# Kernel optimization log

Hardware: AMD Instinct MI355X
Metric: run time of the kernel (lower is better)

## Reference

```python
import jax, jax.numpy as jnp
import numpy as np
import math

B, L, HID = 2, 2048, 1024
H, DK, RATIO, SHARED, TOPK = 4, 64, 4, 1, 2
EXP_V = 2
DV = DK * EXP_V
KEY_DIM = H * DK
VAL_DIM = KEY_DIM * EXP_V
HE = H * RATIO
KS = 4
EPS = 1e-5


def _silu(x):
    return x * jax.nn.sigmoid(x)


def _dwconv_causal(x, w):
    # x: (B, L, C), w: (C, KS); causal depthwise short conv
    xp = jnp.pad(x, ((0, 0), (KS - 1, 0), (0, 0))).transpose(0, 2, 1)
    y = jax.lax.conv_general_dilated(xp, w[:, None, :], (1,), 'VALID',
                                     feature_group_count=w.shape[0],
                                     dimension_numbers=('NCH', 'OIH', 'NCH'))
    return y.transpose(0, 2, 1)


def _l2norm(x):
    return x * jax.lax.rsqrt(jnp.sum(x * x, -1, keepdims=True) + 1e-6)


def _forward(hidden_states, Wq, Wk, Wv, Wb, Wa, Wg, Wo, conv_q, conv_k, conv_v,
             Wq_exp, Wk_exp, W_gate, A_log, dt_bias, norm_w):
    x = hidden_states
    q = _silu(_dwconv_causal(x @ Wq.T, conv_q)).reshape(B, L, H, DK)
    k = _silu(_dwconv_causal(x @ Wk.T, conv_k)).reshape(B, L, H, DK)
    v = _silu(_dwconv_causal(x @ Wv.T, conv_v)).reshape(B, L, H, DV)
    # per-head expert expansion -> (B,L,H,RATIO,DK)
    qe = jnp.einsum('blhd,hkd->blhk', q, Wq_exp).reshape(B, L, H, RATIO, DK)
    ke = jnp.einsum('blhd,hkd->blhk', k, Wk_exp).reshape(B, L, H, RATIO, DK)
    qe = _l2norm(qe) * (DK ** -0.5)
    ke = _l2norm(ke)
    # token-policy top-k routing over non-shared experts
    logits = jnp.einsum('blhd,nd->blhn', q, W_gate)
    scores = jax.nn.softmax(logits.astype(jnp.float32), axis=-1)
    tw, ti = jax.lax.top_k(scores, TOPK)
    tw = tw / jnp.sum(tw, -1, keepdims=True)
    full = jnp.sum(jax.nn.one_hot(ti + SHARED, RATIO, dtype=tw.dtype) * tw[..., None], axis=-2)
    full = full.at[..., :SHARED].set(1.0 / SHARED)
    w_r = (full / jnp.sum(full, -1, keepdims=True)).astype(x.dtype)  # (B,L,H,RATIO)
    mask = (w_r > 0).astype(x.dtype)
    beta = jax.nn.sigmoid(x @ Wb.T).reshape(B, L, H, RATIO) * mask
    g = -jnp.exp(A_log).reshape(H, RATIO) * jax.nn.softplus((x @ Wa.T) + dt_bias).reshape(B, L, H, RATIO)
    g = g * mask  # unrouted memories: exp(0)=1, no decay, no update
    # gated delta-rule recurrence over HE = H*RATIO memories
    qs = qe.reshape(B, L, HE, DK).transpose(1, 0, 2, 3)
    ks_ = ke.reshape(B, L, HE, DK).transpose(1, 0, 2, 3)
    vs = jnp.broadcast_to(v[:, :, :, None, :], (B, L, H, RATIO, DV)).reshape(B, L, HE, DV).transpose(1, 0, 2, 3)
    bs = beta.reshape(B, L, HE).transpose(1, 0, 2)
    gs = g.reshape(B, L, HE).transpose(1, 0, 2)

    def step(S, xs):
        qt, kt, vt, bt, gt = xs
        S = S * jnp.exp(gt)[..., None, None]
        kv = jnp.einsum('bhk,bhkv->bhv', kt, S)
        S = S + jnp.einsum('bhk,bhv->bhkv', kt, (vt - kv) * bt[..., None])
        return S, jnp.einsum('bhk,bhkv->bhv', qt, S)

    S0 = jnp.zeros((B, HE, DK, DV), x.dtype)
    _, o = jax.lax.scan(step, S0, (qs, ks_, vs, bs, gs))
    o = o.transpose(1, 0, 2, 3).reshape(B, L, H, RATIO, DV)
    o = jnp.einsum('blhe,blhev->blhv', w_r, o)
    # FusedRMSNormSwishGate + output projection
    gate = (x @ Wg.T).reshape(B, L, H, DV)
    o = o * jax.lax.rsqrt(jnp.mean(o * o, -1, keepdims=True) + EPS) * norm_w * _silu(gate)
    return o.reshape(B, L, VAL_DIM) @ Wo.T


def setup_inputs():
    keys = jax.random.split(jax.random.key(0), 18)
    n = lambda i, shp, sc=1.0: jax.random.normal(keys[i], shp, jnp.float32) * sc
    A = jax.random.uniform(keys[14], (HE,), jnp.float32, 1e-3, 16.0)
    dt = jnp.exp(jax.random.uniform(keys[15], (HE,), jnp.float32) * (math.log(0.1) - math.log(0.001)) + math.log(0.001))
    dt = jnp.clip(dt, 1e-4, None)
    return {
        'hidden_states': n(0, (B, L, HID)),
        'Wq': n(1, (KEY_DIM, HID), HID ** -0.5),
        'Wk': n(2, (KEY_DIM, HID), HID ** -0.5),
        'Wv': n(3, (VAL_DIM, HID), HID ** -0.5),
        'Wb': n(4, (HE, HID), HID ** -0.5),
        'Wa': n(5, (HE, HID), HID ** -0.5),
        'Wg': n(6, (VAL_DIM, HID), HID ** -0.5),
        'Wo': n(7, (HID, VAL_DIM), VAL_DIM ** -0.5),
        'conv_q': n(8, (KEY_DIM, KS), 0.5),
        'conv_k': n(9, (KEY_DIM, KS), 0.5),
        'conv_v': n(10, (VAL_DIM, KS), 0.5),
        'Wq_exp': n(11, (H, RATIO * DK, DK), DK ** -0.5),
        'Wk_exp': n(12, (H, RATIO * DK, DK), DK ** -0.5),
        'W_gate': n(13, (RATIO - SHARED, DK), DK ** -0.5),
        'A_log': jnp.log(A),
        'dt_bias': dt + jnp.log(-jnp.expm1(-dt)),
        'norm_w': jnp.ones((DV,), jnp.float32),
    }


def reference(hidden_states, Wq, Wk, Wv, Wb, Wa, Wg, Wo, conv_q, conv_k, conv_v,
              Wq_exp, Wk_exp, W_gate, A_log, dt_bias, norm_w):
    return _forward(hidden_states, Wq, Wk, Wv, Wb, Wa, Wg, Wo, conv_q, conv_k, conv_v,
                    Wq_exp, Wk_exp, W_gate, A_log, dt_bias, norm_w)
```

## Files before the change

kernel.cpp:

```cpp
#include <hip/hip_runtime.h>
#include <hip/hip_bf16.h>
#include <math.h>

#define B_    2
#define L_    2048
#define HID_  1024
#define H_    4
#define DK_   64
#define RATIO_ 4
#define HE_   16
#define DV_   128
#define T_    64
#define NC_   32
#define SPITCH 72
#define APITCH 68
#define NCAT  1408
#define QMP   68
#define QMSZ  4352

typedef __attribute__((ext_vector_type(8))) short short8;
typedef __attribute__((ext_vector_type(4))) float f32x4;

__device__ __forceinline__ float sigmoidf_(float x){ return 1.f/(1.f+expf(-x)); }
__device__ __forceinline__ ushort f2bf(float x){
  __hip_bfloat16 h = __float2bfloat16(x);
  return *reinterpret_cast<ushort*>(&h);
}
__device__ __forceinline__ float bf2f(ushort u){
  union { uint32_t i; float f; } v; v.i = ((uint32_t)u) << 16; return v.f;
}

__global__ __launch_bounds__(256) void cast_bf16(const float* __restrict__ in,
                                                 ushort* __restrict__ out, int n)
{
  int i = blockIdx.x*256 + threadIdx.x;
  if (i < n) out[i] = f2bf(in[i]);
}

__global__ __launch_bounds__(256) void concat_wcat(const float* __restrict__ Wk,
    const float* __restrict__ Wv, const float* __restrict__ Wg,
    const float* __restrict__ Wb, const float* __restrict__ Wa,
    ushort* __restrict__ Wcat)
{
  int idx = blockIdx.x*256 + threadIdx.x;
  if (idx >= NCAT*1024) return;
  int r = idx >> 10, cc = idx & 1023;
  float v = 0.f;
  if      (r < 256)  v = Wk[(size_t)r*1024 + cc];
  else if (r < 768)  v = Wv[(size_t)(r-256)*1024 + cc];
  else if (r < 1280) v = Wg[(size_t)(r-768)*1024 + cc];
  else if (r < 1296) v = Wb[(size_t)(r-1280)*1024 + cc];
  else if (r < 1312) v = Wa[(size_t)(r-1296)*1024 + cc];
  Wcat[idx] = f2bf(v);
}

__global__ __launch_bounds__(256) void gemm_bf16(
    const ushort* __restrict__ A, int lda,
    const ushort* __restrict__ Bm, int ldb,
    float* __restrict__ C, int ldc, int K)
{
  __shared__ ushort As[128*32];
  __shared__ ushort Bs[128*32];
  const int tid  = threadIdx.x;
  const int wave = tid >> 6, lane = tid & 63;
  const int row0 = blockIdx.y*128, col0 = blockIdx.x*128;
  const int wr = (wave >> 1) * 64, wc = (wave & 1) * 64;
  const int frow = lane & 15;
  const int fko  = (lane >> 4) << 3;
  f32x4 acc[4][4];
  #pragma unroll
  for (int i=0;i<4;i++)
    #pragma unroll
    for (int j=0;j<4;j++) acc[i][j] = (f32x4){0.f,0.f,0.f,0.f};
  for (int k0 = 0; k0 < K; k0 += 32) {
    #pragma unroll
    for (int cc = 0; cc < 2; cc++) {
      int c  = wave*128 + cc*64 + lane;
      int r  = c >> 2;
      int ko = (c & 3) << 3;
      __builtin_amdgcn_global_load_lds(
        (const __attribute__((address_space(1))) void*)(A + (size_t)(row0+r)*lda + k0 + ko),
        (__attribute__((address_space(3))) void*)(As + (size_t)(wave*128 + cc*64)*8),
        16, 0, 0);
      __builtin_amdgcn_global_load_lds(
        (const __attribute__((address_space(1))) void*)(Bm + (size_t)(col0+r)*ldb + k0 + ko),
        (__attribute__((address_space(3))) void*)(Bs + (size_t)(wave*128 + cc*64)*8),
        16, 0, 0);
    }
    __syncthreads();
    short8 af[4], bfv[4];
    #pragma unroll
    for (int mi=0;mi<4;mi++)
      af[mi] = *reinterpret_cast<const short8*>(&As[(wr + mi*16 + frow)*32 + fko]);
    #pragma unroll
    for (int ni=0;ni<4;ni++)
      bfv[ni] = *reinterpret_cast<const short8*>(&Bs[(wc + ni*16 + frow)*32 + fko]);
    #pragma unroll
    for (int mi=0;mi<4;mi++)
      #pragma unroll
      for (int ni=0;ni<4;ni++)
        acc[mi][ni] = __builtin_amdgcn_mfma_f32_16x16x32_bf16(af[mi], bfv[ni], acc[mi][ni], 0, 0, 0);
    __syncthreads();
  }
  const int ocol = lane & 15;
  const int orow = (lane >> 4) << 2;
  #pragma unroll
  for (int mi=0;mi<4;mi++)
    #pragma unroll
    for (int ni=0;ni<4;ni++) {
      size_t base = (size_t)(row0 + wr + mi*16 + orow)*ldc + (col0 + wc + ni*16 + ocol);
      #pragma unroll
      for (int q=0;q<4;q++) C[base + (size_t)q*ldc] = acc[mi][ni][q];
    }
}

__global__ __launch_bounds__(256) void gemm_expand_bf16(
    const ushort* __restrict__ qc_bf, const ushort* __restrict__ kc_bf,
    const ushort* __restrict__ Wqeb, const ushort* __restrict__ Wkeb,
    ushort* __restrict__ qeb, ushort* __restrict__ keb)
{
  const int z = blockIdx.z;
  const int hh = z & 3;
  const ushort* A  = (z < 4 ? qc_bf : kc_bf) + hh*64;
  const ushort* Bm = (z < 4 ? Wqeb  : Wkeb ) + (size_t)hh*16384;
  ushort* C        = (z < 4 ? qeb   : keb  ) + hh*256;
  const int lda = 256, ldb = 64, ldc = 1024, K = 64;
  __shared__ ushort As[128*32];
  __shared__ ushort Bs[128*32];
  const int tid  = threadIdx.x;
  const int wave = tid >> 6, lane = tid & 63;
  const int row0 = blockIdx.y*128, col0 = blockIdx.x*128;
  const int wr = (wave >> 1) * 64, wc = (wave & 1) * 64;
  const int frow = lane & 15;
  const int fko  = (lane >> 4) << 3;
  f32x4 acc[4][4];
  #pragma unroll
  for (int i=0;i<4;i++)
    #pragma unroll
    for (int j=0;j<4;j++) acc[i][j] = (f32x4){0.f,0.f,0.f,0.f};
  for (int k0 = 0; k0 < K; k0 += 32) {
    #pragma unroll
    for (int cc = 0; cc < 2; cc++) {
      int c  = wave*128 + cc*64 + lane;
      int r  = c >> 2;
      int ko = (c & 3) << 3;
      __builtin_amdgcn_global_load_lds(
        (const __attribute__((address_space(1))) void*)(A + (size_t)(row0+r)*lda + k0 + ko),
        (__attribute__((address_space(3))) void*)(As + (size_t)(wave*128 + cc*64)*8),
        16, 0, 0);
      __builtin_amdgcn_global_load_lds(
        (const __attribute__((address_space(1))) void*)(Bm + (size_t)(col0+r)*ldb + k0 + ko),
        (__attribute__((address_space(3))) void*)(Bs + (size_t)(wave*128 + cc*64)*8),
        16, 0, 0);
    }
    __syncthreads();
    short8 af[4], bfv[4];
    #pragma unroll
    for (int mi=0;mi<4;mi++)
      af[mi] = *reinterpret_cast<const short8*>(&As[(wr + mi*16 + frow)*32 + fko]);
    #pragma unroll
    for (int ni=0;ni<4;ni++)
      bfv[ni] = *reinterpret_cast<const short8*>(&Bs[(wc + ni*16 + frow)*32 + fko]);
    #pragma unroll
    for (int mi=0;mi<4;mi++)
      #pragma unroll
      for (int ni=0;ni<4;ni++)
        acc[mi][ni] = __builtin_amdgcn_mfma_f32_16x16x32_bf16(af[mi], bfv[ni], acc[mi][ni], 0, 0, 0);
    __syncthreads();
  }
  const int ocol = lane & 15;
  const int orow = (lane >> 4) << 2;
  #pragma unroll
  for (int mi=0;mi<4;mi++)
    #pragma unroll
    for (int ni=0;ni<4;ni++) {
      size_t base = (size_t)(row0 + wr + mi*16 + orow)*ldc + (col0 + wc + ni*16 + ocol);
      #pragma unroll
      for (int q=0;q<4;q++) C[base + (size_t)q*ldc] = f2bf(acc[mi][ni][q]);
    }
}

__global__ __launch_bounds__(256) void gemm_f32_db(const float* __restrict__ A, int lda,
    const float* __restrict__ Bm, int ldb, float* __restrict__ C, int ldc,
    int M, int N, int K)
{
  __shared__ float As[2][32][64];
  __shared__ float Bs[2][32][64];
  const int tid = threadIdx.x;
  const int row0 = blockIdx.y * 64;
  const int col0 = blockIdx.x * 64;
  const int tx = tid & 15, ty = tid >> 4;
  const int r0s = tid >> 3;
  const int k4s = (tid & 7) << 2;
  float4 av0, av1, bv0, bv1;

  av0 = *(const float4*)&A[(size_t)(row0 + r0s)*lda + k4s];
  av1 = *(const float4*)&A[(size_t)(row0 + r0s + 32)*lda + k4s];
  bv0 = (col0 + r0s < N) ? *(const float4*)&Bm[(size_t)(col0 + r0s)*ldb + k4s] : make_float4(0,0,0,0);
  bv1 = (col0 + r0s + 32 < N) ? *(const float4*)&Bm[(size_t)(col0 + r0s + 32)*ldb + k4s] : make_float4(0,0,0,0);
  As[0][k4s+0][r0s] = av0.x; As[0][k4s+1][r0s] = av0.y; As[0][k4s+2][r0s] = av0.z; As[0][k4s+3][r0s] = av0.w;
  As[0][k4s+0][r0s+32] = av1.x; As[0][k4s+1][r0s+32] = av1.y; As[0][k4s+2][r0s+32] = av1.z; As[0][k4s+3][r0s+32] = av1.w;
  Bs[0][k4s+0][r0s] = bv0.x; Bs[0][k4s+1][r0s] = bv0.y; Bs[0][k4s+2][r0s] = bv0.z; Bs[0][k4s+3][r0s] = bv0.w;
  Bs[0][k4s+0][r0s+32] = bv1.x; Bs[0][k4s+1][r0s+32] = bv1.y; Bs[0][k4s+2][r0s+32] = bv1.z; Bs[0][k4s+3][r0s+32] = bv1.w;
  __syncthreads();

  float acc[4][4] = {};
  const int nt = K >> 5;
  for (int kt = 0; kt < nt; ++kt) {
    const int p = kt & 1;
    if (kt + 1 < nt) {
      int k0 = (kt+1) << 5;
      av0 = *(const float4*)&A[(size_t)(row0 + r0s)*lda + k0 + k4s];
      av1 = *(const float4*)&A[(size_t)(row0 + r0s + 32)*lda + k0 + k4s];
      bv0 = (col0 + r0s < N) ? *(const float4*)&Bm[(size_t)(col0 + r0s)*ldb + k0 + k4s] : make_float4(0,0,0,0);
      bv1 = (col0 + r0s + 32 < N) ? *(const float4*)&Bm[(size_t)(col0 + r0s + 32)*ldb + k0 + k4s] : make_float4(0,0,0,0);
    }
    #pragma unroll
    for (int kk = 0; kk < 32; kk++) {
      float4 a4 = *(const float4*)&As[p][kk][ty*4];
      float4 b4 = *(const float4*)&Bs[p][kk][tx*4];
      float a[4] = {a4.x,a4.y,a4.z,a4.w};
      float b[4] = {b4.x,b4.y,b4.z,b4.w};
      #pragma unroll
      for (int i=0;i<4;i++)
        #pragma unroll
        for (int j=0;j<4;j++) acc[i][j] += a[i]*b[j];
    }
    if (kt + 1 < nt) {
      const int q = p ^ 1;
      As[q][k4s+0][r0s] = av0.x; As[q][k4s+1][r0s] = av0.y; As[q][k4s+2][r0s] = av0.z; As[q][k4s+3][r0s] = av0.w;
      As[q][k4s+0][r0s+32] = av1.x; As[q][k4s+1][r0s+32] = av1.y; As[q][k4s+2][r0s+32] = av1.z; As[q][k4s+3][r0s+32] = av1.w;
      Bs[q][k4s+0][r0s] = bv0.x; Bs[q][k4s+1][r0s] = bv0.y; Bs[q][k4s+2][r0s] = bv0.z; Bs[q][k4s+3][r0s] = bv0.w;
      Bs[q][k4s+0][r0s+32] = bv1.x; Bs[q][k4s+1][r0s+32] = bv1.y; Bs[q][k4s+2][r0s+32] = bv1.z; Bs[q][k4s+3][r0s+32] = bv1.w;
    }
    __syncthreads();
  }
  #pragma unroll
  for (int i=0;i<4;i++) {
    int r = row0 + ty*4 + i;
    #pragma unroll
    for (int j=0;j<4;j++) {
      int cc = col0 + tx*4 + j;
      if (cc < N) C[(size_t)r*ldc + cc] = acc[i][j];
    }
  }
}

__global__ __launch_bounds__(256) void conv_silu(const float* __restrict__ in, int ild,
    const float* __restrict__ w, float* __restrict__ outf, ushort* __restrict__ outb,
    int C, int total)
{
  int n = blockIdx.x*256 + threadIdx.x;
  if (n >= total) return;
  int c = n % C;
  int t = (n / C) % L_;
  int b = n / (C*L_);
  float acc = 0.f;
  #pragma unroll
  for (int s = 0; s < 4; s++) {
    int tt = t - 3 + s;
    if (tt >= 0) acc += in[((size_t)b*L_ + tt)*ild + c] * w[c*4+s];
  }
  float y = acc * sigmoidf_(acc);
  if (outf) outf[n] = y;
  if (outb) outb[n] = f2bf(y);
}

__global__ __launch_bounds__(256) void routing(const float* __restrict__ qc,
    const float* __restrict__ kvgba, const float* __restrict__ Wg3,
    const float* __restrict__ A_log, const float* __restrict__ dt_bias,
    float* __restrict__ w_buf, float* __restrict__ bt_buf, float* __restrict__ g_buf)
{
  int n = blockIdx.x*256 + threadIdx.x;
  int h  = n & 3;
  int bl = n >> 2;
  const float* q = qc + (size_t)bl*256 + h*64;
  float l0=0.f, l1=0.f, l2=0.f;
  for (int d=0; d<64; d++) {
    float qd = q[d];
    l0 += qd*Wg3[d]; l1 += qd*Wg3[64+d]; l2 += qd*Wg3[128+d];
  }
  float mx = fmaxf(l0, fmaxf(l1, l2));
  float e0 = expf(l0-mx), e1 = expf(l1-mx), e2 = expf(l2-mx);
  float inv_s = 1.f/(e0+e1+e2);
  float p0 = e0*inv_s, p1 = e1*inv_s, p2 = e2*inv_s;
  int m1 = 0; float pm1 = p0;
  if (p1 > pm1) { m1 = 1; pm1 = p1; }
  if (p2 > pm1) { m1 = 2; pm1 = p2; }
  int ia = (m1==0) ? 1 : 0;
  int ib = (m1==2) ? 1 : 2;
  float pa = (m1==0) ? p1 : p0;
  float pb = (m1==2) ? p1 : p2;
  int   m2  = (pb > pa) ? ib : ia;
  float pm2 = (pb > pa) ? pb : pa;
  float inv_w = 1.f/(pm1 + pm2);
  float w1 = 0.5f*pm1*inv_w;
  float w2 = 0.5f*pm2*inv_w;
  #pragma unroll
  for (int r = 0; r < 4; r++) {
    float wr = (r==0) ? 0.5f : (((r-1)==m1) ? w1 : (((r-1)==m2) ? w2 : 0.f));
    int he = h*4 + r;
    size_t gi = (size_t)bl*16 + he;
    w_buf[gi] = wr;
    float mask = (wr > 0.f) ? 1.f : 0.f;
    bt_buf[gi] = mask * sigmoidf_(kvgba[(size_t)bl*NCAT + 1280 + he]);
    float av = kvgba[(size_t)bl*NCAT + 1296 + he] + dt_bias[he];
    float sp = fmaxf(av, 0.f) + log1pf(expf(-fabsf(av)));
    g_buf[gi] = -expf(A_log[he]) * sp * mask;
  }
}

__global__ __launch_bounds__(256) void l2norm_rows_bf(ushort* __restrict__ v, float scale)
{
  int row  = blockIdx.x*4 + (threadIdx.x >> 6);
  int lane = threadIdx.x & 63;
  size_t idx = (size_t)row*64 + lane;
  float x = bf2f(v[idx]);
  float ss = x*x;
  #pragma unroll
  for (int off = 32; off > 0; off >>= 1) ss += __shfl_xor(ss, off);
  v[idx] = f2bf(x * rsqrtf(ss + 1e-6f) * scale);
}

__device__ __forceinline__ f32x4 tile64(const ushort* Am, int r0,
                                        const ushort* Bm, int c0, int lane)
{
  f32x4 acc = {0.f,0.f,0.f,0.f};
  const int fr = lane & 15, fo = (lane >> 4) << 3;
  #pragma unroll
  for (int kk = 0; kk < 2; ++kk) {
    short8 a = *reinterpret_cast<const short8*>(&Am[(r0+fr)*SPITCH + fo + kk*32]);
    short8 b = *reinterpret_cast<const short8*>(&Bm[(c0+fr)*SPITCH + fo + kk*32]);
    acc = __builtin_amdgcn_mfma_f32_16x16x32_bf16(a, b, acc, 0, 0, 0);
  }
  return acc;
}

__global__ __launch_bounds__(256,2) void scan_chunk_mfma(
    const ushort* __restrict__ keb, const ushort* __restrict__ qeb,
    const float* __restrict__ vc, const float* __restrict__ bt_buf,
    const float* __restrict__ g_buf, float* __restrict__ o_r,
    float* __restrict__ Qt, float* __restrict__ Mc, float* __restrict__ Bc)
{
  __shared__ float smem[18496];
  ushort* Kbf = (ushort*)smem;
  ushort* Qbf = (ushort*)(smem + 2304);
  ushort* KTD = (ushort*)(smem + 4608);
  float*  Af  = smem + 6912;
  ushort* Pf  = (ushort*)(smem + 6912);
  ushort* UV  = (ushort*)(smem + 11264);
  float*  cgs = smem + 18176;
  float*  bts = cgs + 64;
  float*  bGs = bts + 64;
  float*  Ds  = bGs + 64;
  float*  gams= Ds + 64;

  const int id = blockIdx.x;
  const int c   = id >> 5;
  const int bhe = id & 31;
  const int b  = bhe >> 4;
  const int he = bhe & 15;
  const int h = he >> 2;
  const int tid = threadIdx.x;
  const int wave = tid >> 6, lane = tid & 63;
  const size_t l0 = (size_t)b*L_ + (size_t)c*T_;

  const int tr = tid >> 2;
  const int sg = tid & 3;
  uint32_t kwv[8], qwv[8];
  float4 vreg[8];
  {
    const uint4* kp = (const uint4*)(keb + (l0+tr)*1024 + he*64 + sg*16);
    const uint4* qp = (const uint4*)(qeb + (l0+tr)*1024 + he*64 + sg*16);
    uint4 k0 = kp[0], k1 = kp[1], q0 = qp[0], q1 = qp[1];
    kwv[0]=k0.x; kwv[1]=k0.y; kwv[2]=k0.z; kwv[3]=k0.w;
    kwv[4]=k1.x; kwv[5]=k1.y; kwv[6]=k1.z; kwv[7]=k1.w;
    qwv[0]=q0.x; qwv[1]=q0.y; qwv[2]=q0.z; qwv[3]=q0.w;
    qwv[4]=q1.x; qwv[5]=q1.y; qwv[6]=q1.z; qwv[7]=q1.w;
    const float4* vp = (const float4*)&vc[(l0+tr)*(H_*DV_) + h*DV_ + sg*32];
    #pragma unroll
    for (int i=0;i<8;i++) vreg[i] = vp[i];
  }
  if (tid < 64) {
    float g  = g_buf[(l0+tid)*HE_ + he];
    float bt = bt_buf[(l0+tid)*HE_ + he];
    float cg = g;
    #pragma unroll
    for (int off = 1; off < 64; off <<= 1) {
      float o = __shfl_up(cg, off);
      if (tid >= off) cg += o;
    }
    float cg63 = __shfl(cg, 63);
    cgs[tid] = cg; bts[tid] = bt;
    float gm = expf(cg);
    gams[tid] = gm; bGs[tid] = bt*gm; Ds[tid] = expf(cg63 - cg);
  }
  __syncthreads();
  {
    float Dt = Ds[tr];
    uint2* kdst = (uint2*)(Kbf + tr*SPITCH + sg*16);
    uint2* qdst = (uint2*)(Qbf + tr*SPITCH + sg*16);
    #pragma unroll
    for (int i=0;i<4;i++){
      kdst[i] = make_uint2(kwv[2*i], kwv[2*i+1]);
      qdst[i] = make_uint2(qwv[2*i], qwv[2*i+1]);
    }
    #pragma unroll
    for (int i=0;i<8;i++){
      ushort lo = (ushort)(kwv[i] & 0xffff), hi = (ushort)(kwv[i] >> 16);
      int d = sg*16 + 2*i;
      KTD[(d+0)*SPITCH + tr] = f2bf(bf2f(lo)*Dt);
      KTD[(d+1)*SPITCH + tr] = f2bf(bf2f(hi)*Dt);
    }
    ushort* Vb = UV;
    #pragma unroll
    for (int i=0;i<8;i++){
      float vv[4] = {vreg[i].x,vreg[i].y,vreg[i].z,vreg[i].w};
      #pragma unroll
      for (int j=0;j<4;j++)
        Vb[tr*128 + sg*32 + i*4 + j] = f2bf(vv[j]);
    }
  }
  __syncthreads();
  {
    const int r0 = wave*16;
    #pragma unroll
    for (int ct=0; ct<4; ++ct) {
      f32x4 acc = tile64(Kbf, r0, Kbf, ct*16, lane);
      int t = r0 + ((lane>>4)<<2);
      int s = ct*16 + (lane&15);
      #pragma unroll
      for (int q=0;q<4;q++){
        int tq = t + q;
        Af[tq*APITCH + s] = (s < tq) ? bts[tq]*expf(cgs[tq]-cgs[s])*acc[q] : 0.f;
      }
    }
  }
  __syncthreads();
  float u[64];
  if (tid < 192) {
    if (tid < 128) {
      const ushort* Vb = UV;
      #pragma unroll
      for (int s=0;s<64;++s) u[s] = bts[s]*bf2f(Vb[s*128 + tid]);
    } else {
      #pragma unroll
      for (int s=0;s<64;++s) u[s] = bGs[s]*bf2f(Kbf[s*SPITCH + (tid-128)]);
    }
  }
  __syncthreads();
  if (tid < 192) {
    #pragma unroll
    for (int t=1;t<64;++t) {
      const float4* Ar = (const float4*)(Af + t*APITCH);
      float p0=0.f,p1=0.f,p2=0.f,p3=0.f;
      #pragma unroll
      for (int s4=0; s4*4<t; ++s4) {
        float4 a = Ar[s4];
        p0 += a.x*u[s4*4+0]; p1 += a.y*u[s4*4+1];
        p2 += a.z*u[s4*4+2]; p3 += a.w*u[s4*4+3];
      }
      u[t] -= (p0+p1)+(p2+p3);
    }
    ushort* Ut = UV;
    uint4* dst = (uint4*)&Ut[tid*SPITCH];
    #pragma unroll
    for (int i=0;i<8;++i) {
      uint32_t w0 = ((uint32_t)f2bf(u[8*i+1])<<16) | f2bf(u[8*i+0]);
      uint32_t w1 = ((uint32_t)f2bf(u[8*i+3])<<16) | f2bf(u[8*i+2]);
      uint32_t w2 = ((uint32_t)f2bf(u[8*i+5])<<16) | f2bf(u[8*i+4]);
      uint32_t w3 = ((uint32_t)f2bf(u[8*i+7])<<16) | f2bf(u[8*i+6]);
      dst[i] = make_uint4(w0,w1,w2,w3);
    }
  }
  __syncthreads();
  {
    const int r0 = wave*16;
    f32x4 accs[4];
    #pragma unroll
    for (int ct=0; ct<4; ++ct) accs[ct] = tile64(Qbf, r0, Kbf, ct*16, lane);
    __syncthreads();
    #pragma unroll
    for (int ct=0; ct<4; ++ct) {
      int t = r0 + ((lane>>4)<<2);
      int s = ct*16 + (lane&15);
      #pragma unroll
      for (int q=0;q<4;q++){
        int tq = t + q;
        float val = (s <= tq) ? expf(cgs[tq]-cgs[s])*accs[ct][q] : 0.f;
        Pf[tq*SPITCH + s] = f2bf(val);
      }
    }
  }
  __syncthreads();
  {
    const int r0 = wave*16;
    const float gend = expf(cgs[63]);
    const ushort* Ut = UV;
    const ushort* UtK = UV + 128*SPITCH;
    const size_t bb = ((size_t)bhe*NC_ + c)*(size_t)(64*128);
    const size_t pb = ((size_t)bhe*NC_ + c)*(size_t)QMSZ;
    #pragma unroll
    for (int jt=0; jt<8; ++jt) {
      f32x4 acc = tile64(Pf, r0, Ut, jt*16, lane);
      int t = r0 + ((lane>>4)<<2);
      int j = jt*16 + (lane&15);
      #pragma unroll
      for (int q=0;q<4;q++)
        o_r[((l0 + t + q)*HE_ + he)*DV_ + j] = acc[q];
    }
    #pragma unroll
    for (int jt=0; jt<8; ++jt) {
      f32x4 acc = tile64(KTD, r0, Ut, jt*16, lane);
      int i = r0 + ((lane>>4)<<2);
      int j = jt*16 + (lane&15);
      #pragma unroll
      for (int q=0;q<4;q++)
        Bc[bb + (size_t)(i+q)*128 + j] = acc[q];
    }
    #pragma unroll
    for (int ct=0; ct<4; ++ct) {
      f32x4 acc = tile64(KTD, r0, UtK, ct*16, lane);
      int i = r0 + ((lane>>4)<<2);
      int m = ct*16 + (lane&15);
      #pragma unroll
      for (int q=0;q<4;q++){
        float val = -acc[q];
        if (i + q == m) val += gend;
        Mc[pb + (size_t)(i+q)*QMP + m] = val;
      }
    }
    #pragma unroll
    for (int ct=0; ct<4; ++ct) {
      f32x4 acc = tile64(Pf, r0, UtK, ct*16, lane);
      int t = r0 + ((lane>>4)<<2);
      int m = ct*16 + (lane&15);
      #pragma unroll
      for (int q=0;q<4;q++)
        Qt[pb + (size_t)(t+q)*QMP + m] = gams[t+q]*bf2f(Qbf[(t+q)*SPITCH + m]) - acc[q];
    }
  }
}

__device__ __forceinline__ void stage_qm(const float* __restrict__ src, float* dst,
                                         int wave, int lane)
{
  #pragma unroll
  for (int pass = 0; pass < 4; ++pass){
    int cb = pass*256 + wave*64;
    __builtin_amdgcn_global_load_lds(
      (const __attribute__((address_space(1))) void*)(src + (size_t)(cb+lane)*4),
      (__attribute__((address_space(3))) void*)(dst + cb*4), 16, 0, 0);
  }
  if (wave == 0)
    __builtin_amdgcn_global_load_lds(
      (const __attribute__((address_space(1))) void*)(src + 4096 + (size_t)lane*4),
      (__attribute__((address_space(3))) void*)(dst + 4096), 16, 0, 0);
}

__global__ __launch_bounds__(256) void compose_correct(
    const float* __restrict__ Mc, const float* __restrict__ Bc,
    const float* __restrict__ Qt, float* __restrict__ o_r)
{
  __shared__ float Ql[2][4352];
  __shared__ float Ml[2][4352];
  __shared__ float SSl[1024];
  const int bhe = blockIdx.x;
  const int j0  = blockIdx.y * 16;
  const int b = bhe >> 4, he = bhe & 15;
  const int tid = threadIdx.x;
  const int wave = tid >> 6, lane = tid & 63;
  const int rw = tid >> 2;
  const int jg = tid & 3;

  for (int id = tid; id < 1024; id += 256) SSl[id] = 0.f;

  stage_qm(Mc + (size_t)(bhe*NC_)*QMSZ, Ml[0], wave, lane);
  float4 bcur = *(const float4*)&Bc[(size_t)(bhe*NC_)*8192 + rw*128 + j0 + jg*4];
  __syncthreads();

  int p = 0;
  for (int c = 0; c < NC_; ++c){
    float4 bnext = make_float4(0.f,0.f,0.f,0.f);
    if (c+1 < NC_){
      stage_qm(Qt + (size_t)(bhe*NC_ + c + 1)*QMSZ, Ql[p^1], wave, lane);
      if (c+1 < NC_-1){
        stage_qm(Mc + (size_t)(bhe*NC_ + c + 1)*QMSZ, Ml[p^1], wave, lane);
        bnext = *(const float4*)&Bc[(size_t)(bhe*NC_ + c + 1)*8192 + rw*128 + j0 + jg*4];
      }
    }
    const float4* SS4 = (const float4*)SSl;
    if (c > 0){
      float4 oa = make_float4(0.f,0.f,0.f,0.f);
      const float* Qr = Ql[p] + rw*QMP;
      #pragma unroll
      for (int m = 0; m < 64; m += 4){
        float4 qv = *(const float4*)&Qr[m];
        float4 s0 = SS4[(m+0)*4 + jg];
        float4 s1 = SS4[(m+1)*4 + jg];
        float4 s2 = SS4[(m+2)*4 + jg];
        float4 s3 = SS4[(m+3)*4 + jg];
        oa.x += qv.x*s0.x + qv.y*s1.x + qv.z*s2.x + qv.w*s3.x;
        oa.y += qv.x*s0.y + qv.y*s1.y + qv.z*s2.y + qv.w*s3.y;
        oa.z += qv.x*s0.z + qv.y*s1.z + qv.z*s2.z + qv.w*s3.z;
        oa.w += qv.x*s0.w + qv.y*s1.w + qv.z*s2.w + qv.w*s3.w;
      }
      size_t oi = (((size_t)b*L_ + c*T_ + rw)*HE_ + he)*DV_ + j0 + jg*4;
      float4 o = *(float4*)&o_r[oi];
      o.x += oa.x; o.y += oa.y; o.z += oa.z; o.w += oa.w;
      *(float4*)&o_r[oi] = o;
    }
    float4 ns = bcur;
    if (c < NC_-1){
      const float* Mr = Ml[p] + rw*QMP;
      #pragma unroll
      for (int m = 0; m < 64; m += 4){
        float4 mv = *(const float4*)&Mr[m];
        float4 s0 = SS4[(m+0)*4 + jg];
        float4 s1 = SS4[(m+1)*4 + jg];
        float4 s2 = SS4[(m+2)*4 + jg];
        float4 s3 = SS4[(m+3)*4 + jg];
        ns.x += mv.x*s0.x + mv.y*s1.x + mv.z*s2.x + mv.w*s3.x;
        ns.y += mv.x*s0.y + mv.y*s1.y + mv.z*s2.y + mv.w*s3.y;
        ns.z += mv.x*s0.z + mv.y*s1.z + mv.z*s2.z + mv.w*s3.z;
        ns.w += mv.x*s0.w + mv.y*s1.w + mv.z*s2.w + mv.w*s3.w;
      }
    }
    __syncthreads();
    if (c < NC_-1) *(float4*)&SSl[rw*16 + jg*4] = ns;
    __syncthreads();
    p ^= 1;
    bcur = bnext;
  }
}

__global__ __launch_bounds__(128) void combine(const float* __restrict__ o_r,
    const float* __restrict__ w_buf, const float* __restrict__ kvgba,
    const float* __restrict__ norm_w, ushort* __restrict__ o_fin)
{
  int n  = blockIdx.x;
  int h  = n & 3;
  int bl = n >> 2;
  int j  = threadIdx.x;
  size_t wb = (size_t)bl*16 + h*4;
  size_t ob = wb*128 + j;
  float oc = 0.f;
  #pragma unroll
  for (int r = 0; r < 4; r++) oc += w_buf[wb+r] * o_r[ob + (size_t)r*128];
  float ss = oc*oc;
  #pragma unroll
  for (int off = 32; off > 0; off >>= 1) ss += __shfl_xor(ss, off);
  __shared__ float red[2];
  if ((threadIdx.x & 63) == 0) red[threadIdx.x >> 6] = ss;
  __syncthreads();
  float mean = (red[0] + red[1]) * (1.f/128.f);
  float sc = rsqrtf(mean + 1e-5f);
  float gv = kvgba[(size_t)bl*NCAT + 768 + h*128 + j];
  o_fin[(size_t)bl*512 + h*128 + j] = f2bf(oc * sc * norm_w[j] * (gv * sigmoidf_(gv)));
}

extern "C" void kernel_launch(void* const* d_in, const int* in_sizes, int n_in,
                              void* d_out, int out_size, void* d_ws, size_t ws_size,
                              hipStream_t stream)
{
  (void)in_sizes; (void)n_in; (void)out_size; (void)ws_size;
  const float* x       = (const float*)d_in[0];
  const float* Wq      = (const float*)d_in[1];
  const float* Wk      = (const float*)d_in[2];
  const float* Wv      = (const float*)d_in[3];
  const float* Wb      = (const float*)d_in[4];
  const float* Wa      = (const float*)d_in[5];
  const float* Wg      = (const float*)d_in[6];
  const float* Wo      = (const float*)d_in[7];
  const float* conv_q  = (const float*)d_in[8];
  const float* conv_k  = (const float*)d_in[9];
  const float* conv_v  = (const float*)d_in[10];
  const float* Wq_exp  = (const float*)d_in[11];
  const float* Wk_exp  = (const float*)d_in[12];
  const float* W_gate  = (const float*)d_in[13];
  const float* A_log   = (const float*)d_in[14];
  const float* dt_bias = (const float*)d_in[15];
  const float* norm_w  = (const float*)d_in[16];
  float* out = (float*)d_out;

  const size_t BL = (size_t)B_*L_;
  float* p = (float*)d_ws;
  float* q_lin  = p; p += BL*256;
  float* kvgba  = p; p += BL*NCAT;
  float* q_conv = p; p += BL*256;
  float* v_conv = p; p += BL*512;
  float* w_buf  = p; p += BL*16;
  float* bt_buf = p; p += BL*16;
  float* g_buf  = p; p += BL*16;
  float* Mc     = p; p += (size_t)B_*HE_*NC_*QMSZ + 256;
  float* Bc     = p; p += (size_t)B_*HE_*NC_*64*128;
  float* Qt     = p; p += (size_t)B_*HE_*NC_*QMSZ + 256;
  float* o_r    = p; p += BL*16*128;
  ushort* xb    = (ushort*)p; p += BL*512;
  ushort* Wcat  = (ushort*)p; p += (NCAT*1024)/2;
  ushort* qc_bf = (ushort*)p; p += BL*128;
  ushort* kc_bf = (ushort*)p; p += BL*128;
  ushort* qeb   = (ushort*)p; p += BL*512;
  ushort* keb   = (ushort*)p; p += BL*512;
  ushort* Wqeb  = (ushort*)p; p += 32768;
  ushort* Wkeb  = (ushort*)p; p += 32768;
  ushort* Wob   = (ushort*)p; p += 262144;
  ushort* o_finb= (ushort*)p; p += BL*256;

  concat_wcat<<<dim3((NCAT*1024+255)/256), dim3(256), 0, stream>>>(Wk, Wv, Wg, Wb, Wa, Wcat);
  { int n = (int)(BL*1024); cast_bf16<<<dim3((n+255)/256), dim3(256), 0, stream>>>(x, xb, n); }
  { int n = 65536;  cast_bf16<<<dim3((n+255)/256), dim3(256), 0, stream>>>(Wq_exp, Wqeb, n); }
  { int n = 65536;  cast_bf16<<<dim3((n+255)/256), dim3(256), 0, stream>>>(Wk_exp, Wkeb, n); }
  { int n = 524288; cast_bf16<<<dim3((n+255)/256), dim3(256), 0, stream>>>(Wo, Wob, n); }

  gemm_f32_db<<<dim3(4, 64), dim3(256), 0, stream>>>(x, 1024, Wq, 1024, q_lin, 256, 4096, 256, 1024);
  gemm_bf16<<<dim3(NCAT/128, 32), dim3(256), 0, stream>>>(xb, 1024, Wcat, 1024, kvgba, NCAT, 1024);

  { int tot = B_*L_*256; conv_silu<<<dim3((tot+255)/256), dim3(256), 0, stream>>>(q_lin, 256, conv_q, q_conv, qc_bf, 256, tot); }
  { int tot = B_*L_*256; conv_silu<<<dim3((tot+255)/256), dim3(256), 0, stream>>>(kvgba, NCAT, conv_k, (float*)nullptr, kc_bf, 256, tot); }
  { int tot = B_*L_*512; conv_silu<<<dim3((tot+255)/256), dim3(256), 0, stream>>>(kvgba + 256, NCAT, conv_v, v_conv, (ushort*)nullptr, 512, tot); }

  routing<<<dim3(64), dim3(256), 0, stream>>>(q_conv, kvgba, W_gate, A_log, dt_bias,
                                              w_buf, bt_buf, g_buf);

  gemm_expand_bf16<<<dim3(2, 32, 8), dim3(256), 0, stream>>>(qc_bf, kc_bf, Wqeb, Wkeb, qeb, keb);

  l2norm_rows_bf<<<dim3(16384), dim3(256), 0, stream>>>(qeb, 0.125f);
  l2norm_rows_bf<<<dim3(16384), dim3(256), 0, stream>>>(keb, 1.0f);

  scan_chunk_mfma<<<dim3(NC_*HE_*B_), dim3(256), 0, stream>>>(keb, qeb, v_conv, bt_buf, g_buf,
                                                              o_r, Qt, Mc, Bc);
  compose_correct<<<dim3(32, 8), dim3(256), 0, stream>>>(Mc, Bc, Qt, o_r);
  combine<<<dim3(B_*L_*H_), dim3(128), 0, stream>>>(o_r, w_buf, kvgba, norm_w, o_finb);

  gemm_bf16<<<dim3(8, 32), dim3(256), 0, stream>>>(o_finb, 512, Wob, 512, out, 1024, 512);
}
```

Measured before the change: 372.0 us.

## Store chunk intermediates Mc/Qt/Bc and conv'd V in bf16 with XOR swizzle

Changes the per-chunk transition matrices Mc, Qt and Bc written by the chunk scan to bf16, and has the V conv output go straight to bf16 instead of fp32. The Q/M tiles drop their padded pitch and use an XOR-swizzled 64-wide layout to avoid LDS bank conflicts, and compose_correct stages half as many bytes per chunk. The aim is to halve global traffic between the scan and compose kernels and cut the LDS footprint. The cost is lower precision in the state-propagation matrices, which may add accuracy error across the 32-chunk composition.

Result: faster. 360.9 us (-3.0%).

```diff
diff --git a/kernel.cpp b/kernel.cpp
--- a/kernel.cpp
+++ b/kernel.cpp
@@ -15,8 +15,6 @@
 #define SPITCH 72
 #define APITCH 68
 #define NCAT  1408
-#define QMP   68
-#define QMSZ  4352
 
 typedef __attribute__((ext_vector_type(8))) short short8;
 typedef __attribute__((ext_vector_type(4))) float f32x4;
@@ -28,6 +26,12 @@
 }
 __device__ __forceinline__ float bf2f(ushort u){
   union { uint32_t i; float f; } v; v.i = ((uint32_t)u) << 16; return v.f;
+}
+__device__ __forceinline__ void unpk8(uint4 w, float* f){
+  f[0]=bf2f((ushort)(w.x&0xffff)); f[1]=bf2f((ushort)(w.x>>16));
+  f[2]=bf2f((ushort)(w.y&0xffff)); f[3]=bf2f((ushort)(w.y>>16));
+  f[4]=bf2f((ushort)(w.z&0xffff)); f[5]=bf2f((ushort)(w.z>>16));
+  f[6]=bf2f((ushort)(w.w&0xffff)); f[7]=bf2f((ushort)(w.w>>16));
 }
 
 __global__ __launch_bounds__(256) void cast_bf16(const float* __restrict__ in,
@@ -338,9 +342,9 @@
 
 __global__ __launch_bounds__(256,2) void scan_chunk_mfma(
     const ushort* __restrict__ keb, const ushort* __restrict__ qeb,
-    const float* __restrict__ vc, const float* __restrict__ bt_buf,
+    const ushort* __restrict__ vcb, const float* __restrict__ bt_buf,
     const float* __restrict__ g_buf, float* __restrict__ o_r,
-    float* __restrict__ Qt, float* __restrict__ Mc, float* __restrict__ Bc)
+    ushort* __restrict__ Qtb, ushort* __restrict__ Mcb, ushort* __restrict__ Bcb)
 {
   __shared__ float smem[18496];
   ushort* Kbf = (ushort*)smem;
@@ -368,7 +372,7 @@
   const int tr = tid >> 2;
   const int sg = tid & 3;
   uint32_t kwv[8], qwv[8];
-  float4 vreg[8];
+  uint4 vw0, vw1, vw2, vw3;
   {
     const uint4* kp = (const uint4*)(keb + (l0+tr)*1024 + he*64 + sg*16);
     const uint4* qp = (const uint4*)(qeb + (l0+tr)*1024 + he*64 + sg*16);
@@ -377,9 +381,8 @@
     kwv[4]=k1.x; kwv[5]=k1.y; kwv[6]=k1.z; kwv[7]=k1.w;
     qwv[0]=q0.x; qwv[1]=q0.y; qwv[2]=q0.z; qwv[3]=q0.w;
     qwv[4]=q1.x; qwv[5]=q1.y; qwv[6]=q1.z; qwv[7]=q1.w;
-    const float4* vp = (const float4*)&vc[(l0+tr)*(H_*DV_) + h*DV_ + sg*32];
-    #pragma unroll
-    for (int i=0;i<8;i++) vreg[i] = vp[i];
+    const uint4* vp = (const uint4*)(vcb + (l0+tr)*512 + h*128 + sg*32);
+    vw0 = vp[0]; vw1 = vp[1]; vw2 = vp[2]; vw3 = vp[3];
   }
   if (tid < 64) {
     float g  = g_buf[(l0+tid)*HE_ + he];
@@ -412,14 +415,8 @@
       KTD[(d+0)*SPITCH + tr] = f2bf(bf2f(lo)*Dt);
       KTD[(d+1)*SPITCH + tr] = f2bf(bf2f(hi)*Dt);
     }
-    ushort* Vb = UV;
-    #pragma unroll
-    for (int i=0;i<8;i++){
-      float vv[4] = {vreg[i].x,vreg[i].y,vreg[i].z,vreg[i].w};
-      #pragma unroll
-      for (int j=0;j<4;j++)
-        Vb[tr*128 + sg*32 + i*4 + j] = f2bf(vv[j]);
-    }
+    uint4* vdst = (uint4*)(UV + tr*128 + sg*32);
+    vdst[0] = vw0; vdst[1] = vw1; vdst[2] = vw2; vdst[3] = vw3;
   }
   __syncthreads();
   {
@@ -499,7 +496,7 @@
     const ushort* Ut = UV;
     const ushort* UtK = UV + 128*SPITCH;
     const size_t bb = ((size_t)bhe*NC_ + c)*(size_t)(64*128);
-    const size_t pb = ((size_t)bhe*NC_ + c)*(size_t)QMSZ;
+    const size_t pb = ((size_t)bhe*NC_ + c)*(size_t)(64*64);
     #pragma unroll
     for (int jt=0; jt<8; ++jt) {
       f32x4 acc = tile64(Pf, r0, Ut, jt*16, lane);
@@ -516,7 +513,7 @@
       int j = jt*16 + (lane&15);
       #pragma unroll
       for (int q=0;q<4;q++)
-        Bc[bb + (size_t)(i+q)*128 + j] = acc[q];
+        Bcb[bb + (size_t)(i+q)*128 + j] = f2bf(acc[q]);
     }
     #pragma unroll
     for (int ct=0; ct<4; ++ct) {
@@ -526,8 +523,10 @@
       #pragma unroll
       for (int q=0;q<4;q++){
         float val = -acc[q];
-        if (i + q == m) val += gend;
-        Mc[pb + (size_t)(i+q)*QMP + m] = val;
+        int row = i + q;
+        if (row == m) val += gend;
+        int pc = (((m>>3)^(row&7))<<3) | (m&7);
+        Mcb[pb + (size_t)row*64 + pc] = f2bf(val);
       }
     }
     #pragma unroll
@@ -536,34 +535,33 @@
       int t = r0 + ((lane>>4)<<2);
       int m = ct*16 + (lane&15);
       #pragma unroll
-      for (int q=0;q<4;q++)
-        Qt[pb + (size_t)(t+q)*QMP + m] = gams[t+q]*bf2f(Qbf[(t+q)*SPITCH + m]) - acc[q];
-    }
-  }
-}
-
-__device__ __forceinline__ void stage_qm(const float* __restrict__ src, float* dst,
+      for (int q=0;q<4;q++){
+        int row = t + q;
+        int pc = (((m>>3)^(row&7))<<3) | (m&7);
+        Qtb[pb + (size_t)row*64 + pc] = f2bf(gams[row]*bf2f(Qbf[row*SPITCH + m]) - acc[q]);
+      }
+    }
+  }
+}
+
+__device__ __forceinline__ void stage_qm(const ushort* __restrict__ src, ushort* dst,
                                          int wave, int lane)
 {
   #pragma unroll
-  for (int pass = 0; pass < 4; ++pass){
-    int cb = pass*256 + wave*64;
+  for (int pass = 0; pass < 2; ++pass){
+    int idx = pass*256 + wave*64 + lane;
     __builtin_amdgcn_global_load_lds(
-      (const __attribute__((address_space(1))) void*)(src + (size_t)(cb+lane)*4),
-      (__attribute__((address_space(3))) void*)(dst + cb*4), 16, 0, 0);
-  }
-  if (wave == 0)
-    __builtin_amdgcn_global_load_lds(
-      (const __attribute__((address_space(1))) void*)(src + 4096 + (size_t)lane*4),
-      (__attribute__((address_space(3))) void*)(dst + 4096), 16, 0, 0);
+      (const __attribute__((address_space(1))) void*)(src + (size_t)idx*8),
+      (__attribute__((address_space(3))) void*)(dst + (size_t)idx*8), 16, 0, 0);
+  }
 }
 
 __global__ __launch_bounds__(256) void compose_correct(
-    const float* __restrict__ Mc, const float* __restrict__ Bc,
-    const float* __restrict__ Qt, float* __restrict__ o_r)
-{
-  __shared__ float Ql[2][4352];
-  __shared__ float Ml[2][4352];
+    const ushort* __restrict__ Mcb, const ushort* __restrict__ Bcb,
+    const ushort* __restrict__ Qtb, float* __restrict__ o_r)
+{
+  __shared__ ushort Ql[2][4096];
+  __shared__ ushort Ml[2][4096];
   __shared__ float SSl[1024];
   const int bhe = blockIdx.x;
   const int j0  = blockIdx.y * 16;
@@ -572,38 +570,44 @@
   const int wave = tid >> 6, lane = tid & 63;
   const int rw = tid >> 2;
   const int jg = tid & 3;
+  const int rsw = rw & 7;
 
   for (int id = tid; id < 1024; id += 256) SSl[id] = 0.f;
 
-  stage_qm(Mc + (size_t)(bhe*NC_)*QMSZ, Ml[0], wave, lane);
-  float4 bcur = *(const float4*)&Bc[(size_t)(bhe*NC_)*8192 + rw*128 + j0 + jg*4];
+  stage_qm(Mcb + (size_t)(bhe*NC_)*4096, Ml[0], wave, lane);
+  float4 bcur;
+  {
+    uint2 bw = *(const uint2*)&Bcb[(size_t)(bhe*NC_)*8192 + rw*128 + j0 + jg*4];
+    bcur = make_float4(bf2f((ushort)(bw.x&0xffff)), bf2f((ushort)(bw.x>>16)),
+                       bf2f((ushort)(bw.y&0xffff)), bf2f((ushort)(bw.y>>16)));
+  }
   __syncthreads();
 
   int p = 0;
   for (int c = 0; c < NC_; ++c){
     float4 bnext = make_float4(0.f,0.f,0.f,0.f);
     if (c+1 < NC_){
-      stage_qm(Qt + (size_t)(bhe*NC_ + c + 1)*QMSZ, Ql[p^1], wave, lane);
+      stage_qm(Qtb + (size_t)(bhe*NC_ + c + 1)*4096, Ql[p^1], wave, lane);
       if (c+1 < NC_-1){
-        stage_qm(Mc + (size_t)(bhe*NC_ + c + 1)*QMSZ, Ml[p^1], wave, lane);
-        bnext = *(const float4*)&Bc[(size_t)(bhe*NC_ + c + 1)*8192 + rw*128 + j0 + jg*4];
+        stage_qm(Mcb + (size_t)(bhe*NC_ + c + 1)*4096, Ml[p^1], wave, lane);
+        uint2 bw = *(const uint2*)&Bcb[(size_t)(bhe*NC_ + c + 1)*8192 + rw*128 + j0 + jg*4];
+        bnext = make_float4(bf2f((ushort)(bw.x&0xffff)), bf2f((ushort)(bw.x>>16)),
+                            bf2f((ushort)(bw.y&0xffff)), bf2f((ushort)(bw.y>>16)));
       }
     }
     const float4* SS4 = (const float4*)SSl;
     if (c > 0){
       float4 oa = make_float4(0.f,0.f,0.f,0.f);
-      const float* Qr = Ql[p] + rw*QMP;
-      #pragma unroll
-      for (int m = 0; m < 64; m += 4){
-        float4 qv = *(const float4*)&Qr[m];
-        float4 s0 = SS4[(m+0)*4 + jg];
-        float4 s1 = SS4[(m+1)*4 + jg];
-        float4 s2 = SS4[(m+2)*4 + jg];
-        float4 s3 = SS4[(m+3)*4 + jg];
-        oa.x += qv.x*s0.x + qv.y*s1.x + qv.z*s2.x + qv.w*s3.x;
-        oa.y += qv.x*s0.y + qv.y*s1.y + qv.z*s2.y + qv.w*s3.y;
-        oa.z += qv.x*s0.z + qv.y*s1.z + qv.z*s2.z + qv.w*s3.z;
-        oa.w += qv.x*s0.w + qv.y*s1.w + qv.z*s2.w + qv.w*s3.w;
+      const ushort* Qr = Ql[p] + rw*64;
+      #pragma unroll
+      for (int gb = 0; gb < 8; ++gb){
+        uint4 w = *(const uint4*)&Qr[(gb ^ rsw) << 3];
+        float f[8]; unpk8(w, f);
+        #pragma unroll
+        for (int e = 0; e < 8; ++e){
+          float4 s = SS4[(gb*8+e)*4 + jg];
+          oa.x += f[e]*s.x; oa.y += f[e]*s.y; oa.z += f[e]*s.z; oa.w += f[e]*s.w;
+        }
       }
       size_t oi = (((size_t)b*L_ + c*T_ + rw)*HE_ + he)*DV_ + j0 + jg*4;
       float4 o = *(float4*)&o_r[oi];
@@ -612,18 +616,16 @@
     }
     float4 ns = bcur;
     if (c < NC_-1){
-      const float* Mr = Ml[p] + rw*QMP;
-      #pragma unroll
-      for (int m = 0; m < 64; m += 4){
-        float4 mv = *(const float4*)&Mr[m];
-        float4 s0 = SS4[(m+0)*4 + jg];
-        float4 s1 = SS4[(m+1)*4 + jg];
-        float4 s2 = SS4[(m+2)*4 + jg];
-        float4 s3 = SS4[(m+3)*4 + jg];
-        ns.x += mv.x*s0.x + mv.y*s1.x + mv.z*s2.x + mv.w*s3.x;
-        ns.y += mv.x*s0.y + mv.y*s1.y + mv.z*s2.y + mv.w*s3.y;
-        ns.z += mv.x*s0.z + mv.y*s1.z + mv.z*s2.z + mv.w*s3.z;
-        ns.w += mv.x*s0.w + mv.y*s1.w + mv.z*s2.w + mv.w*s3.w;
+      const ushort* Mr = Ml[p] + rw*64;
+      #pragma unroll
+      for (int gb = 0; gb < 8; ++gb){
+        uint4 w = *(const uint4*)&Mr[(gb ^ rsw) << 3];
+        float f[8]; unpk8(w, f);
+        #pragma unroll
+        for (int e = 0; e < 8; ++e){
+          float4 s = SS4[(gb*8+e)*4 + jg];
+          ns.x += f[e]*s.x; ns.y += f[e]*s.y; ns.z += f[e]*s.z; ns.w += f[e]*s.w;
+        }
       }
     }
     __syncthreads();
@@ -688,14 +690,14 @@
   float* q_lin  = p; p += BL*256;
   float* kvgba  = p; p += BL*NCAT;
   float* q_conv = p; p += BL*256;
-  float* v_conv = p; p += BL*512;
   float* w_buf  = p; p += BL*16;
   float* bt_buf = p; p += BL*16;
   float* g_buf  = p; p += BL*16;
-  float* Mc     = p; p += (size_t)B_*HE_*NC_*QMSZ + 256;
-  float* Bc     = p; p += (size_t)B_*HE_*NC_*64*128;
-  float* Qt     = p; p += (size_t)B_*HE_*NC_*QMSZ + 256;
   float* o_r    = p; p += BL*16*128;
+  ushort* Mcb   = (ushort*)p; p += (size_t)B_*HE_*NC_*2048;
+  ushort* Qtb   = (ushort*)p; p += (size_t)B_*HE_*NC_*2048;
+  ushort* Bcb   = (ushort*)p; p += (size_t)B_*HE_*NC_*4096;
+  ushort* v_convb=(ushort*)p; p += BL*256;
   ushort* xb    = (ushort*)p; p += BL*512;
   ushort* Wcat  = (ushort*)p; p += (NCAT*1024)/2;
   ushort* qc_bf = (ushort*)p; p += BL*128;
@@ -718,7 +720,7 @@
 
   { int tot = B_*L_*256; conv_silu<<<dim3((tot+255)/256), dim3(256), 0, stream>>>(q_lin, 256, conv_q, q_conv, qc_bf, 256, tot); }
   { int tot = B_*L_*256; conv_silu<<<dim3((tot+255)/256), dim3(256), 0, stream>>>(kvgba, NCAT, conv_k, (float*)nullptr, kc_bf, 256, tot); }
-  { int tot = B_*L_*512; conv_silu<<<dim3((tot+255)/256), dim3(256), 0, stream>>>(kvgba + 256, NCAT, conv_v, v_conv, (ushort*)nullptr, 512, tot); }
+  { int tot = B_*L_*512; conv_silu<<<dim3((tot+255)/256), dim3(256), 0, stream>>>(kvgba + 256, NCAT, conv_v, (float*)nullptr, v_convb, 512, tot); }
 
   routing<<<dim3(64), dim3(256), 0, stream>>>(q_conv, kvgba, W_gate, A_log, dt_bias,
                                               w_buf, bt_buf, g_buf);
@@ -728,9 +730,9 @@
   l2norm_rows_bf<<<dim3(16384), dim3(256), 0, stream>>>(qeb, 0.125f);
   l2norm_rows_bf<<<dim3(16384), dim3(256), 0, stream>>>(keb, 1.0f);
 
-  scan_chunk_mfma<<<dim3(NC_*HE_*B_), dim3(256), 0, stream>>>(keb, qeb, v_conv, bt_buf, g_buf,
-                                                              o_r, Qt, Mc, Bc);
-  compose_correct<<<dim3(32, 8), dim3(256), 0, stream>>>(Mc, Bc, Qt, o_r);
+  scan_chunk_mfma<<<dim3(NC_*HE_*B_), dim3(256), 0, stream>>>(keb, qeb, v_convb, bt_buf, g_buf,
+                                                              o_r, Qtb, Mcb, Bcb);
+  compose_correct<<<dim3(32, 8), dim3(256), 0, stream>>>(Mcb, Bcb, Qtb, o_r);
   combine<<<dim3(B_*L_*H_), dim3(128), 0, stream>>>(o_r, w_buf, kvgba, norm_w, o_finb);
 
   gemm_bf16<<<dim3(8, 32), dim3(256), 0, stream>>>(o_finb, 512, Wob, 512, out, 1024, 512);
```
